# Performance work log

Hardware: AMD Instinct MI355X
Metric: run time of the kernel (lower is better)

## Reference

```python
import jax, jax.numpy as jnp
import numpy as np

B, P, L = 8, 196, 80
DIM1, DIM2, ATT = 2048, 300, 1024


def setup_inputs() -> dict:
    key = jax.random.key(0)
    ks = jax.random.split(key, 8)
    s1 = 1.0 / np.sqrt(DIM1)
    s2 = 1.0 / np.sqrt(DIM2)
    sa = 1.0 / np.sqrt(ATT)
    return {
        "x1": jax.random.normal(ks[0], (B, P, DIM1), dtype=jnp.float32),
        "x2": jax.random.normal(ks[1], (B, L, DIM2), dtype=jnp.float32),
        "W1": jax.random.uniform(ks[2], (DIM1, ATT), jnp.float32, -s1, s1),
        "W2": jax.random.uniform(ks[3], (DIM2, ATT), jnp.float32, -s2, s2),
        "Wh": jax.random.uniform(ks[4], (ATT, ATT), jnp.float32, -sa, sa),
        "bh": jax.random.uniform(ks[5], (ATT,), jnp.float32, -sa, sa),
        "Wt": jax.random.uniform(ks[6], (ATT,), jnp.float32, -sa, sa),
        "bt": jax.random.uniform(ks[7], (), jnp.float32, -sa, sa),
    }


def reference(x1, x2, W1, W2, Wh, bh, Wt, bt):
    # linear1 / linear2 (no bias)
    a1 = jnp.einsum('bpd,da->bpa', x1, W1)            # (B, P, ATT)
    a2 = jnp.einsum('bld,da->bla', x2, W2)            # (B, L, ATT)
    u = jnp.tanh(a1[:, None, :, :] * a2[:, :, None, :])  # (B, L, P, ATT)
    # target_linear(hidden_linear(u)) folded: u @ (Wh @ Wt) + (bh @ Wt + bt)
    w = Wh @ Wt                                        # (ATT,)
    score = jnp.einsum('blpa,a->blp', u, w) + (bh @ Wt + bt)  # (B, L, P)
    alpha = jax.nn.softmax(score, axis=-1)             # (B, L, P)
    label_repr = jnp.einsum('blp,bpd->bld', alpha, x1)  # (B, L, DIM1)
    return (label_repr, alpha)
```

## Files before the change

kernel.cpp:

```cpp
#include <hip/hip_runtime.h>
#include <math.h>

#define B_   8
#define P_   196
#define L_   80
#define DIM1 2048
#define DIM2 300
#define ATT  1024

typedef __attribute__((ext_vector_type(8))) short short8_t;
typedef __attribute__((ext_vector_type(4))) float f32x4_t;

__device__ inline unsigned short f2bf(float f) {
    unsigned int u = __float_as_uint(f);
    u += 0x7fff + ((u >> 16) & 1);
    return (unsigned short)(u >> 16);
}
__device__ inline float bf2f(unsigned short h) {
    return __uint_as_float(((unsigned int)h) << 16);
}

__global__ __launch_bounds__(256) void prep_w(const float* __restrict__ Wh,
                                              const float* __restrict__ bh,
                                              const float* __restrict__ Wt,
                                              const float* __restrict__ btp,
                                              float* __restrict__ w,
                                              float* __restrict__ biasp) {
    const int tid  = threadIdx.x;
    const int lane = tid & 63;
    const int row  = blockIdx.x * 4 + (tid >> 6);
    const float* src = (row < ATT) ? (Wh + (size_t)row * ATT) : bh;
    if (row <= ATT) {
        float acc = 0.0f;
#pragma unroll
        for (int it = 0; it < ATT / 256; ++it) {
            const int i = it * 256 + lane * 4;
            const float4 a = *reinterpret_cast<const float4*>(src + i);
            const float4 b = *reinterpret_cast<const float4*>(Wt + i);
            acc = fmaf(a.x, b.x, acc);
            acc = fmaf(a.y, b.y, acc);
            acc = fmaf(a.z, b.z, acc);
            acc = fmaf(a.w, b.w, acc);
        }
#pragma unroll
        for (int o = 32; o >= 1; o >>= 1) acc += __shfl_xor(acc, o);
        if (lane == 0) {
            if (row < ATT) w[row] = acc;
            else           biasp[0] = acc + btp[0];
        }
    }
}

__global__ __launch_bounds__(256) void prep_sum(const float* __restrict__ w,
                                                float* __restrict__ biasp) {
    __shared__ float red[4];
    const int tid = threadIdx.x;
    float s = 0.f;
    for (int i = tid; i < ATT; i += 256) s += w[i];
#pragma unroll
    for (int o = 32; o >= 1; o >>= 1) s += __shfl_xor(s, o);
    if ((tid & 63) == 0) red[tid >> 6] = s;
    __syncthreads();
    if (tid == 0) biasp[1] = biasp[0] + red[0] + red[1] + red[2] + red[3];
}

__global__ __launch_bounds__(256) void tcast(const float* __restrict__ in,
                                             unsigned short* __restrict__ out,
                                             int Ksrc, int Kpad) {
    __shared__ unsigned short tile[32][34];
    const int tx = threadIdx.x & 31, ty = threadIdx.x >> 5;
    const int k0 = blockIdx.x * 32, n0 = blockIdx.y * 32;
#pragma unroll
    for (int i = 0; i < 4; ++i) {
        const int r = k0 + ty + i * 8;
        const float v = (r < Ksrc) ? in[(size_t)r * 1024 + n0 + tx] : 0.f;
        tile[ty + i * 8][tx] = f2bf(v);
    }
    __syncthreads();
#pragma unroll
    for (int i = 0; i < 4; ++i) {
        const int n = ty + i * 8;
        out[(size_t)(n0 + n) * Kpad + k0 + tx] = tile[tx][n];
    }
}

template<int KSRC, int KPAD>
__global__ __launch_bounds__(256) void gemm_bf16(const float* __restrict__ Af,
                                                 const unsigned short* __restrict__ Bt,
                                                 unsigned short* __restrict__ C,
                                                 int M) {
    constexpr int NT = KPAD / 64;
    __shared__ __align__(16) char smem[32768];
    const int tid  = threadIdx.x;
    const int lane = tid & 63;
    const int wave = tid >> 6;
    const int wm = (wave >> 1) * 32;
    const int wn = (wave & 1) * 32;
    const int m0 = blockIdx.y * 64;
    const int n0 = blockIdx.x * 64;

    const int row = tid >> 2;
    const int kc  = (tid & 3) * 16;
    const int swz = (row & 7) << 4;
    const int sb  = row * 128 + kc * 2;
    const int gm  = m0 + row;

    float4   ra[4];
    short8_t rb[2];

    auto LOAD = [&](int t) {
        const int k0 = t * 64;
        if (gm < M && k0 + 64 <= KSRC) {
            const float* ap = Af + (size_t)gm * KSRC + k0 + kc;
            ra[0] = *reinterpret_cast<const float4*>(ap);
            ra[1] = *reinterpret_cast<const float4*>(ap + 4);
            ra[2] = *reinterpret_cast<const float4*>(ap + 8);
            ra[3] = *reinterpret_cast<const float4*>(ap + 12);
        } else {
            float* rf = reinterpret_cast<float*>(ra);
#pragma unroll
            for (int j = 0; j < 16; ++j) {
                const int k = k0 + kc + j;
                rf[j] = (gm < M && k < KSRC) ? Af[(size_t)gm * KSRC + k] : 0.f;
            }
        }
        const unsigned short* bp = Bt + (size_t)(n0 + row) * KPAD + k0 + kc;
        rb[0] = *reinterpret_cast<const short8_t*>(bp);
        rb[1] = *reinterpret_cast<const short8_t*>(bp + 8);
    };

    auto WRITE = [&](int buf) {
        char* smA = smem + buf * 16384;
        char* smB = smA + 8192;
        const float* rf = reinterpret_cast<const float*>(ra);
        short8_t h0, h1;
#pragma unroll
        for (int j = 0; j < 8; ++j) h0[j] = (short)f2bf(rf[j]);
#pragma unroll
        for (int j = 0; j < 8; ++j) h1[j] = (short)f2bf(rf[8 + j]);
        *reinterpret_cast<short8_t*>(smA + ((sb)      ^ swz)) = h0;
        *reinterpret_cast<short8_t*>(smA + ((sb + 16) ^ swz)) = h1;
        *reinterpret_cast<short8_t*>(smB + ((sb)      ^ swz)) = rb[0];
        *reinterpret_cast<short8_t*>(smB + ((sb + 16) ^ swz)) = rb[1];
    };

    f32x4_t acc[2][2] = {};
    const int fr_col = (lane >> 4) << 4;
    const int fl     = lane & 15;

    LOAD(0);
#pragma unroll 2
    for (int t = 0; t < NT; ++t) {
        const int buf = t & 1;
        WRITE(buf);
        __syncthreads();
        if (t + 1 < NT) LOAD(t + 1);
        const char* smA = smem + buf * 16384;
        const char* smB = smA + 8192;
#pragma unroll
        for (int kk = 0; kk < 2; ++kk) {
            short8_t af[2], bf[2];
#pragma unroll
            for (int i = 0; i < 2; ++i) {
                const int r = wm + i * 16 + fl;
                af[i] = *reinterpret_cast<const short8_t*>(
                    smA + ((r * 128 + kk * 64 + fr_col) ^ ((r & 7) << 4)));
            }
#pragma unroll
            for (int j = 0; j < 2; ++j) {
                const int r = wn + j * 16 + fl;
                bf[j] = *reinterpret_cast<const short8_t*>(
                    smB + ((r * 128 + kk * 64 + fr_col) ^ ((r & 7) << 4)));
            }
#pragma unroll
            for (int i = 0; i < 2; ++i)
#pragma unroll
                for (int j = 0; j < 2; ++j)
                    acc[i][j] = __builtin_amdgcn_mfma_f32_16x16x32_bf16(af[i], bf[j], acc[i][j], 0, 0, 0);
        }
        __syncthreads();
    }

#pragma unroll
    for (int i = 0; i < 2; ++i) {
        const int gmb = m0 + wm + i * 16 + ((lane >> 4) << 2);
#pragma unroll
        for (int j = 0; j < 2; ++j) {
            const int gn = n0 + wn + j * 16 + fl;
#pragma unroll
            for (int q = 0; q < 4; ++q) {
                const int gmq = gmb + q;
                if (gmq < M) C[(size_t)gmq * 1024 + gn] = f2bf(acc[i][j][q]);
            }
        }
    }
}

__global__ __launch_bounds__(256) void score_part(const unsigned short* __restrict__ a1b,
                                                  const unsigned short* __restrict__ a2b,
                                                  const float* __restrict__ w,
                                                  const float* __restrict__ biasp,
                                                  float* __restrict__ scb) {
    __shared__ float2 aw[ATT];
    const int tid  = threadIdx.x;
    const int lane = tid & 63;
    const int wave = tid >> 6;
    const int b    = blockIdx.x & 7;
    const int rest = blockIdx.x >> 3;
    const int l    = rest >> 2;
    const int qtr  = rest & 3;
    const float bias2 = biasp[1];

    const unsigned short* a2p = a2b + (size_t)(b * L_ + l) * ATT;
    for (int i = tid; i < ATT; i += 256) {
        const float a2v = bf2f(a2p[i]);
        const int li = i & 511;
        const int phi = (i & ~511) | (((li & 7) << 6) + (li >> 3));
        aw[phi] = make_float2(a2v * 2.885390082f, w[i]);
    }
    __syncthreads();

    const int base = qtr * 49;
    float* scp = scb + (size_t)(b * L_ + l) * P_;

    for (int g = wave; g < 13; g += 4) {
        const int p0 = base + g * 4;
        int r[4];
#pragma unroll
        for (int q = 0; q < 4; ++q) r[q] = min(p0 + q, P_ - 1);
        float acc[4] = {0.f, 0.f, 0.f, 0.f};
#pragma unroll
        for (int it = 0; it < 2; ++it) {
            short8_t v[4];
#pragma unroll
            for (int q = 0; q < 4; ++q)
                v[q] = *reinterpret_cast<const short8_t*>(
                    a1b + (size_t)(b * P_ + r[q]) * ATT + it * 512 + lane * 8);
#pragma unroll
            for (int j = 0; j < 8; ++j) {
                const float2 c = aw[it * 512 + j * 64 + lane];
#pragma unroll
                for (int q = 0; q < 4; ++q) {
                    const float f = bf2f((unsigned short)v[q][j]);
                    const float e = __builtin_amdgcn_exp2f(f * c.x);
                    const float rr = __builtin_amdgcn_rcpf(e + 1.0f);
                    acc[q] = fmaf(c.y, rr, acc[q]);
                }
            }
        }
#pragma unroll
        for (int o = 32; o >= 1; o >>= 1) {
#pragma unroll
            for (int q = 0; q < 4; ++q) acc[q] += __shfl_xor(acc[q], o);
        }
        if (lane < 4) {
            const int p = p0 + lane;
            if (p < base + 49) scp[p] = bias2 - 2.0f * acc[lane];
        }
    }
}

__global__ __launch_bounds__(256) void softmax_k(const float* __restrict__ scb,
                                                 float* __restrict__ alpha) {
    const int tid  = threadIdx.x;
    const int lane = tid & 63;
    const int wave = tid >> 6;
    const int row  = blockIdx.x * 4 + wave;
    const float* sp = scb + (size_t)row * P_;

    float v[4];
#pragma unroll
    for (int k = 0; k < 4; ++k) {
        const int p = lane + k * 64;
        v[k] = (p < P_) ? sp[p] : -INFINITY;
    }
    float m = fmaxf(fmaxf(v[0], v[1]), fmaxf(v[2], v[3]));
#pragma unroll
    for (int o = 32; o >= 1; o >>= 1) m = fmaxf(m, __shfl_xor(m, o));

    float e[4];
    float s = 0.f;
#pragma unroll
    for (int k = 0; k < 4; ++k) {
        const int p = lane + k * 64;
        e[k] = (p < P_) ? __expf(v[k] - m) : 0.f;
        s += e[k];
    }
#pragma unroll
    for (int o = 32; o >= 1; o >>= 1) s += __shfl_xor(s, o);
    const float inv = 1.0f / s;

    float* ap = alpha + (size_t)row * P_;
#pragma unroll
    for (int k = 0; k < 4; ++k) {
        const int p = lane + k * 64;
        if (p < P_) ap[p] = e[k] * inv;
    }
}

#define LT 4
#define DT 512
__global__ __launch_bounds__(256) void label_kernel(const float* __restrict__ alpha,
                                                    const float* __restrict__ x1,
                                                    float* __restrict__ out) {
    __shared__ float al[P_][LT];
    const int tid = threadIdx.x;
    const int b  = blockIdx.z;
    const int l0 = blockIdx.y * LT;
    const int d0 = blockIdx.x * DT;

    for (int idx = tid; idx < P_ * LT; idx += 256) {
        const int p = idx >> 2;
        const int l = idx & 3;
        al[p][l] = alpha[((size_t)(b * L_ + l0 + l)) * P_ + p];
    }
    __syncthreads();

    const int d = d0 + tid * 2;
    float acc[LT][2] = {};
    for (int p = 0; p < P_; ++p) {
        const float2 x = *reinterpret_cast<const float2*>(x1 + ((size_t)(b * P_ + p)) * DIM1 + d);
        const float4 a4 = *reinterpret_cast<const float4*>(&al[p][0]);
        acc[0][0] = fmaf(a4.x, x.x, acc[0][0]);
        acc[0][1] = fmaf(a4.x, x.y, acc[0][1]);
        acc[1][0] = fmaf(a4.y, x.x, acc[1][0]);
        acc[1][1] = fmaf(a4.y, x.y, acc[1][1]);
        acc[2][0] = fmaf(a4.z, x.x, acc[2][0]);
        acc[2][1] = fmaf(a4.z, x.y, acc[2][1]);
        acc[3][0] = fmaf(a4.w, x.x, acc[3][0]);
        acc[3][1] = fmaf(a4.w, x.y, acc[3][1]);
    }
#pragma unroll
    for (int l = 0; l < LT; ++l) {
        float* op = out + ((size_t)(b * L_ + l0 + l)) * DIM1 + d;
        op[0] = acc[l][0];
        op[1] = acc[l][1];
    }
}

extern "C" void kernel_launch(void* const* d_in, const int* in_sizes, int n_in,
                              void* d_out, int out_size, void* d_ws, size_t ws_size,
                              hipStream_t stream) {
    const float* x1 = (const float*)d_in[0];
    const float* x2 = (const float*)d_in[1];
    const float* W1 = (const float*)d_in[2];
    const float* W2 = (const float*)d_in[3];
    const float* Wh = (const float*)d_in[4];
    const float* bh = (const float*)d_in[5];
    const float* Wt = (const float*)d_in[6];
    const float* bt = (const float*)d_in[7];

    float* out       = (float*)d_out;
    float* label_out = out;
    float* alpha_out = out + (size_t)B_ * L_ * DIM1;

    unsigned short* usw = (unsigned short*)d_ws;
    unsigned short* W1T = usw;
    unsigned short* a2b = usw;
    unsigned short* W2T = usw + 2097152;
    unsigned short* a1b = usw + 2424832;
    float* wv    = (float*)(usw + 4030464);
    float* biasv = wv + ATT;
    float* scb   = wv + 1028;

    prep_w<<<ATT / 4 + 1, 256, 0, stream>>>(Wh, bh, Wt, bt, wv, biasv);
    prep_sum<<<1, 256, 0, stream>>>(wv, biasv);

    tcast<<<dim3(DIM1 / 32, 32), 256, 0, stream>>>(W1, W1T, DIM1, DIM1);
    tcast<<<dim3(320 / 32, 32), 256, 0, stream>>>(W2, W2T, DIM2, 320);

    gemm_bf16<DIM1, DIM1><<<dim3(16, 25), 256, 0, stream>>>(x1, W1T, a1b, B_ * P_);
    gemm_bf16<DIM2, 320><<<dim3(16, 10), 256, 0, stream>>>(x2, W2T, a2b, B_ * L_);

    score_part<<<B_ * L_ * 4, 256, 0, stream>>>(a1b, a2b, wv, biasv, scb);
    softmax_k<<<B_ * L_ / 4, 256, 0, stream>>>(scb, alpha_out);

    label_kernel<<<dim3(DIM1 / DT, L_ / LT, B_), 256, 0, stream>>>(
        alpha_out, x1, label_out);
}
```

Measured before the change: 192.2 us.

## Merge prep and transpose kernels, fuse softmax into label kernel, unpack bf16 pairs

The prep_sum pass is dropped: prep_w now accumulates the bias sum with atomics after a memset. The two tcast launches are merged into one grid, and the softmax is fused into the label kernel, which recomputes softmax per d-tile and writes alpha only from the first tile. The score loop unpacks bf16 pairs straight from 32-bit words. This cuts launch count and one global round trip for alpha, at the cost of computing the softmax four times and adding float atomics that make the bias summation order nondeterministic.

```diff
diff --git a/kernel.cpp b/kernel.cpp
--- a/kernel.cpp
+++ b/kernel.cpp
@@ -45,31 +45,34 @@
 #pragma unroll
         for (int o = 32; o >= 1; o >>= 1) acc += __shfl_xor(acc, o);
         if (lane == 0) {
-            if (row < ATT) w[row] = acc;
-            else           biasp[0] = acc + btp[0];
-        }
-    }
-}
-
-__global__ __launch_bounds__(256) void prep_sum(const float* __restrict__ w,
-                                                float* __restrict__ biasp) {
-    __shared__ float red[4];
-    const int tid = threadIdx.x;
-    float s = 0.f;
-    for (int i = tid; i < ATT; i += 256) s += w[i];
-#pragma unroll
-    for (int o = 32; o >= 1; o >>= 1) s += __shfl_xor(s, o);
-    if ((tid & 63) == 0) red[tid >> 6] = s;
-    __syncthreads();
-    if (tid == 0) biasp[1] = biasp[0] + red[0] + red[1] + red[2] + red[3];
-}
-
-__global__ __launch_bounds__(256) void tcast(const float* __restrict__ in,
-                                             unsigned short* __restrict__ out,
-                                             int Ksrc, int Kpad) {
+            if (row < ATT) {
+                w[row] = acc;
+                atomicAdd(&biasp[1], acc);
+            } else {
+                atomicAdd(&biasp[1], acc + btp[0]);
+            }
+        }
+    }
+}
+
+__global__ __launch_bounds__(256) void tcast_all(const float* __restrict__ W1,
+                                                 const float* __restrict__ W2,
+                                                 unsigned short* __restrict__ W1T,
+                                                 unsigned short* __restrict__ W2T) {
     __shared__ unsigned short tile[32][34];
+    int id = blockIdx.x;
+    const float* in;
+    unsigned short* out;
+    int Ksrc, Kpad, k0, n0;
+    if (id < 2048) {
+        in = W1; out = W1T; Ksrc = DIM1; Kpad = DIM1;
+        k0 = (id & 63) * 32; n0 = (id >> 6) * 32;
+    } else {
+        id -= 2048;
+        in = W2; out = W2T; Ksrc = DIM2; Kpad = 320;
+        k0 = (id % 10) * 32; n0 = (id / 10) * 32;
+    }
     const int tx = threadIdx.x & 31, ty = threadIdx.x >> 5;
-    const int k0 = blockIdx.x * 32, n0 = blockIdx.y * 32;
 #pragma unroll
     for (int i = 0; i < 4; ++i) {
         const int r = k0 + ty + i * 8;
@@ -231,20 +234,24 @@
         float acc[4] = {0.f, 0.f, 0.f, 0.f};
 #pragma unroll
         for (int it = 0; it < 2; ++it) {
-            short8_t v[4];
+            uint4 v[4];
 #pragma unroll
             for (int q = 0; q < 4; ++q)
-                v[q] = *reinterpret_cast<const short8_t*>(
+                v[q] = *reinterpret_cast<const uint4*>(
                     a1b + (size_t)(b * P_ + r[q]) * ATT + it * 512 + lane * 8);
 #pragma unroll
-            for (int j = 0; j < 8; ++j) {
-                const float2 c = aw[it * 512 + j * 64 + lane];
+            for (int h = 0; h < 4; ++h) {
+                const float2 c0 = aw[it * 512 + (2 * h + 0) * 64 + lane];
+                const float2 c1 = aw[it * 512 + (2 * h + 1) * 64 + lane];
 #pragma unroll
                 for (int q = 0; q < 4; ++q) {
-                    const float f = bf2f((unsigned short)v[q][j]);
-                    const float e = __builtin_amdgcn_exp2f(f * c.x);
-                    const float rr = __builtin_amdgcn_rcpf(e + 1.0f);
-                    acc[q] = fmaf(c.y, rr, acc[q]);
+                    const unsigned int u = (&v[q].x)[h];
+                    const float flo = __uint_as_float(u << 16);
+                    const float fhi = __uint_as_float(u & 0xffff0000u);
+                    const float elo = __builtin_amdgcn_exp2f(flo * c0.x);
+                    acc[q] = fmaf(c0.y, __builtin_amdgcn_rcpf(elo + 1.0f), acc[q]);
+                    const float ehi = __builtin_amdgcn_exp2f(fhi * c1.x);
+                    acc[q] = fmaf(c1.y, __builtin_amdgcn_rcpf(ehi + 1.0f), acc[q]);
                 }
             }
         }
@@ -260,14 +267,23 @@
     }
 }
 
-__global__ __launch_bounds__(256) void softmax_k(const float* __restrict__ scb,
-                                                 float* __restrict__ alpha) {
+__global__ __launch_bounds__(256) void label_fused(const float* __restrict__ scb,
+                                                   const float* __restrict__ x1,
+                                                   float* __restrict__ alpha,
+                                                   float* __restrict__ out) {
+    __shared__ float al[P_][4];
     const int tid  = threadIdx.x;
     const int lane = tid & 63;
     const int wave = tid >> 6;
-    const int row  = blockIdx.x * 4 + wave;
+    const int id   = blockIdx.x;
+    const int b    = id & 7;
+    const int rest = id >> 3;
+    const int dtile = rest & 3;
+    const int l0    = (rest >> 2) * 4;
+    const int d0    = dtile * 512;
+    const int row   = b * L_ + l0 + wave;
+
     const float* sp = scb + (size_t)row * P_;
-
     float v[4];
 #pragma unroll
     for (int k = 0; k < 4; ++k) {
@@ -277,7 +293,6 @@
     float m = fmaxf(fmaxf(v[0], v[1]), fmaxf(v[2], v[3]));
 #pragma unroll
     for (int o = 32; o >= 1; o >>= 1) m = fmaxf(m, __shfl_xor(m, o));
-
     float e[4];
     float s = 0.f;
 #pragma unroll
@@ -289,35 +304,20 @@
 #pragma unroll
     for (int o = 32; o >= 1; o >>= 1) s += __shfl_xor(s, o);
     const float inv = 1.0f / s;
-
     float* ap = alpha + (size_t)row * P_;
 #pragma unroll
     for (int k = 0; k < 4; ++k) {
         const int p = lane + k * 64;
-        if (p < P_) ap[p] = e[k] * inv;
-    }
-}
-
-#define LT 4
-#define DT 512
-__global__ __launch_bounds__(256) void label_kernel(const float* __restrict__ alpha,
-                                                    const float* __restrict__ x1,
-                                                    float* __restrict__ out) {
-    __shared__ float al[P_][LT];
-    const int tid = threadIdx.x;
-    const int b  = blockIdx.z;
-    const int l0 = blockIdx.y * LT;
-    const int d0 = blockIdx.x * DT;
-
-    for (int idx = tid; idx < P_ * LT; idx += 256) {
-        const int p = idx >> 2;
-        const int l = idx & 3;
-        al[p][l] = alpha[((size_t)(b * L_ + l0 + l)) * P_ + p];
+        if (p < P_) {
+            const float a = e[k] * inv;
+            al[p][wave] = a;
+            if (dtile == 0) ap[p] = a;
+        }
     }
     __syncthreads();
 
     const int d = d0 + tid * 2;
-    float acc[LT][2] = {};
+    float acc[4][2] = {};
     for (int p = 0; p < P_; ++p) {
         const float2 x = *reinterpret_cast<const float2*>(x1 + ((size_t)(b * P_ + p)) * DIM1 + d);
         const float4 a4 = *reinterpret_cast<const float4*>(&al[p][0]);
@@ -331,10 +331,9 @@
         acc[3][1] = fmaf(a4.w, x.y, acc[3][1]);
     }
 #pragma unroll
-    for (int l = 0; l < LT; ++l) {
+    for (int l = 0; l < 4; ++l) {
         float* op = out + ((size_t)(b * L_ + l0 + l)) * DIM1 + d;
-        op[0] = acc[l][0];
-        op[1] = acc[l][1];
+        *reinterpret_cast<float2*>(op) = make_float2(acc[l][0], acc[l][1]);
     }
 }
 
@@ -363,18 +362,16 @@
     float* biasv = wv + ATT;
     float* scb   = wv + 1028;
 
+    hipMemsetAsync(biasv, 0, 2 * sizeof(float), stream);
+
     prep_w<<<ATT / 4 + 1, 256, 0, stream>>>(Wh, bh, Wt, bt, wv, biasv);
-    prep_sum<<<1, 256, 0, stream>>>(wv, biasv);
-
-    tcast<<<dim3(DIM1 / 32, 32), 256, 0, stream>>>(W1, W1T, DIM1, DIM1);
-    tcast<<<dim3(320 / 32, 32), 256, 0, stream>>>(W2, W2T, DIM2, 320);
+
+    tcast_all<<<2048 + 320, 256, 0, stream>>>(W1, W2, W1T, W2T);
 
     gemm_bf16<DIM1, DIM1><<<dim3(16, 25), 256, 0, stream>>>(x1, W1T, a1b, B_ * P_);
     gemm_bf16<DIM2, 320><<<dim3(16, 10), 256, 0, stream>>>(x2, W2T, a2b, B_ * L_);
 
     score_part<<<B_ * L_ * 4, 256, 0, stream>>>(a1b, a2b, wv, biasv, scb);
-    softmax_k<<<B_ * L_ / 4, 256, 0, stream>>>(scb, alpha_out);
-
-    label_kernel<<<dim3(DIM1 / DT, L_ / LT, B_), 256, 0, stream>>>(
-        alpha_out, x1, label_out);
-}
+
+    label_fused<<<B_ * L_ * 4 / 4, 256, 0, stream>>>(scb, x1, alpha_out, label_out);
+}
```

Result: slower. 197.6 us (+2.8%).
